# Performance work log

Measured on AMD Instinct MI355X. Metric: run time of the kernel, lower is better.

Reference implementation:

```python
import jax, jax.numpy as jnp
import numpy as np

N, E, IN, H, OUT = 100000, 600000, 128, 128, 64
BN_EPS = 1e-5


def setup_inputs() -> dict:
    key = jax.random.key(0)
    ks = jax.random.split(key, 8)
    def lin(k, i, o):
        return jax.random.normal(k, (i, o), jnp.float32) / np.float32(np.sqrt(i))
    return {
        "x": jax.random.normal(ks[0], (N, IN), jnp.float32),
        "edge_index": jax.random.randint(ks[1], (2, E), 0, N, dtype=jnp.int64),
        "W1": lin(ks[2], IN, H), "b1": jnp.zeros((H,), jnp.float32),
        "gamma": jnp.ones((H,), jnp.float32), "beta": jnp.zeros((H,), jnp.float32),
        "W2": lin(ks[3], H, H), "b2": jnp.zeros((H,), jnp.float32),
        "Wm1": lin(ks[4], H, H), "bm1": jnp.zeros((H,), jnp.float32),
        "Wm2": lin(ks[5], H, OUT), "bm2": jnp.zeros((OUT,), jnp.float32),
    }


def reference(x, edge_index, W1, b1, gamma, beta, W2, b2, Wm1, bm1, Wm2, bm2):
    # GINConv: h = MLP((1 + eps) * x + sum_{j in N(i)} x_j), eps = 0 (train_eps=False)
    src = edge_index[0]
    dst = edge_index[1]  # PyG aggregates messages at edge_index[1]
    agg = jax.ops.segment_sum(x[src], dst, num_segments=x.shape[0])  # [N, IN]
    h = agg + x
    # inner MLP: Linear -> BatchNorm (batch stats) -> ReLU -> Linear
    h = h @ W1 + b1
    mean = jnp.mean(h, axis=0)
    var = jnp.var(h, axis=0)
    h = (h - mean) * jax.lax.rsqrt(var + BN_EPS) * gamma + beta
    h = jax.nn.relu(h)
    h = h @ W2 + b2
    h = jax.nn.relu(h)  # .relu() after conv
    # output MLP (norm=None, dropout=0.5 -> identity at inference): Linear -> ReLU -> Linear
    h = jax.nn.relu(h @ Wm1 + bm1)
    return h @ Wm2 + bm2
```

## Files before the change

kernel.cpp:

```cpp
#include <hip/hip_runtime.h>
#include <hip/hip_bf16.h>
#include <stdint.h>

#define NNODES 100000
#define NEDGES 600000
#define SCAN_CHUNK 1024
#define SCAN_NB 98

typedef __attribute__((ext_vector_type(8))) short bf16x8;
typedef __attribute__((ext_vector_type(4))) float f32x4;
typedef __attribute__((ext_vector_type(4))) unsigned int u32x4;

__device__ inline float b2f(short b) {
    union { unsigned u; float f; } v;
    v.u = ((unsigned)(unsigned short)b) << 16;
    return v.f;
}
__device__ inline short f2b(float f) {
    union { float f; unsigned u; } v;
    v.f = f;
    unsigned r = (v.u + 0x7FFFu + ((v.u >> 16) & 1u)) >> 16;
    return (short)r;
}
__device__ inline unsigned packbf(float lo, float hi) {
    return ((unsigned)(unsigned short)f2b(hi) << 16) | (unsigned)(unsigned short)f2b(lo);
}
#define MFMA16(a, b, c) __builtin_amdgcn_mfma_f32_16x16x32_bf16(a, b, c, 0, 0, 0)

__device__ inline void stage_lds(const short* __restrict__ g, short* s, int w, int l, int n) {
#pragma unroll
    for (int i = 0; i < n; ++i) {
        int base = i * 4096 + w * 1024;
        __builtin_amdgcn_global_load_lds(
            (const __attribute__((address_space(1))) void*)((const char*)g + base + l * 16),
            (__attribute__((address_space(3))) void*)((char*)s + base), 16, 0, 0);
    }
}

__global__ __launch_bounds__(256) void k_prep(const float* __restrict__ x,
                                              const float* __restrict__ W1,
                                              const float* __restrict__ W2,
                                              const float* __restrict__ Wm1,
                                              const float* __restrict__ Wm2,
                                              short* __restrict__ xb, short* __restrict__ Wt,
                                              int* __restrict__ pos, float* __restrict__ stats) {
    int i = blockIdx.x * 256 + threadIdx.x;
    if (i < (NNODES + 1) * 16) {
        bf16x8 o = (bf16x8){0, 0, 0, 0, 0, 0, 0, 0};
        if (i < NNODES * 16) {
            const float4* p = (const float4*)(x + (size_t)i * 8);
            float4 a = p[0], b = p[1];
            o[0] = f2b(a.x); o[1] = f2b(a.y); o[2] = f2b(a.z); o[3] = f2b(a.w);
            o[4] = f2b(b.x); o[5] = f2b(b.y); o[6] = f2b(b.z); o[7] = f2b(b.w);
        }
        *(bf16x8*)(xb + (size_t)i * 8) = o;
    }
    if (i < NNODES) pos[i] = 0;
    if (i < 57344) {
        int jj, lane, kt, ct;
        const float* W;
        int ldw, off;
        if (i < 16384) { off = i; W = W1; ldw = 128; }
        else if (i < 32768) { off = i - 16384; W = W2; ldw = 128; }
        else if (i < 49152) { off = i - 32768; W = Wm1; ldw = 128; }
        else { off = i - 49152; W = Wm2; ldw = 64; }
        jj = off & 7;
        lane = (off >> 3) & 63;
        kt = (off >> 9) & 3;
        ct = (off >> 11) & 7;
        int lr = lane & 15, hi = lane >> 4;
        int c = ct * 16 + lr;
        int k = kt * 32 + hi * 8 + jj;
        Wt[i] = f2b(W[k * ldw + c]);
    }
    if (i < 256) stats[i] = 0.0f;
}


__global__ __launch_bounds__(256) void k_hist(const int* __restrict__ ei, int* __restrict__ cnt) {
    int e = blockIdx.x * 256 + threadIdx.x;
    if (e < NEDGES) atomicAdd(&cnt[ei[NEDGES + e]], 1);
}

__global__ __launch_bounds__(256) void k_scan1(const int* __restrict__ cnt, int* __restrict__ bsums) {
    __shared__ int sd[256];
    int b = blockIdx.x, t = threadIdx.x;
    int base = b * SCAN_CHUNK + t * 4;
    int s = 0;
#pragma unroll
    for (int i = 0; i < 4; ++i) {
        int idx = base + i;
        if (idx < NNODES) s += cnt[idx];
    }
    sd[t] = s;
    __syncthreads();
    for (int off = 128; off > 0; off >>= 1) {
        if (t < off) sd[t] += sd[t + off];
        __syncthreads();
    }
    if (t == 0) bsums[b] = sd[0];
}

__global__ __launch_bounds__(64) void k_scan2(int* __restrict__ bsums, int* __restrict__ rowptr) {
    if (threadIdx.x == 0 && blockIdx.x == 0) {
        int run = 0;
        for (int b = 0; b < SCAN_NB; ++b) {
            int v = bsums[b];
            bsums[b] = run;
            run += v;
        }
        rowptr[NNODES] = run;
    }
}

__global__ __launch_bounds__(256) void k_scan3(const int* __restrict__ cnt,
                                               const int* __restrict__ bsums,
                                               int* __restrict__ rowptr, int* __restrict__ pos) {
    __shared__ int sd[256];
    int b = blockIdx.x, t = threadIdx.x;
    int base = b * SCAN_CHUNK + t * 4;
    int v[4];
    int s = 0;
#pragma unroll
    for (int i = 0; i < 4; ++i) {
        int idx = base + i;
        v[i] = (idx < NNODES) ? cnt[idx] : 0;
        s += v[i];
    }
    sd[t] = s;
    __syncthreads();
    for (int off = 1; off < 256; off <<= 1) {
        int val = (t >= off) ? sd[t - off] : 0;
        __syncthreads();
        sd[t] += val;
        __syncthreads();
    }
    int run = sd[t] - s + bsums[b];
#pragma unroll
    for (int i = 0; i < 4; ++i) {
        int idx = base + i;
        if (idx < NNODES) {
            rowptr[idx] = run;
            pos[idx] = run;
            run += v[i];
        }
    }
}

__global__ __launch_bounds__(256) void k_fill(const int* __restrict__ ei, int* __restrict__ pos,
                                              int* __restrict__ elist) {
    int e = blockIdx.x * 256 + threadIdx.x;
    if (e >= NEDGES) return;
    int src = ei[e];
    int dst = ei[NEDGES + e];
    int p = atomicAdd(&pos[dst], 1);
    elist[p] = src;
}

__global__ __launch_bounds__(256) void k_agg(const short* __restrict__ xb,
                                             const int* __restrict__ rowptr,
                                             const int* __restrict__ elist,
                                             short* __restrict__ bufb) {
    int t = threadIdx.x;
    int w = t >> 6, lane = t & 63;
    int node = blockIdx.x * 4 + w;
    if (node >= NNODES) return;
    int beg = rowptr[node];
    int end = rowptr[node + 1];
    int deg = end - beg;
    int total = deg + 1;
    int sub = lane & 31, half = lane >> 5;
    const uint2* xr = (const uint2*)xb;

    float acc0 = 0.f, acc1 = 0.f, acc2 = 0.f, acc3 = 0.f;

    for (int base = 0; base < total; base += 64) {
        int j = base + lane;
        int ej = NNODES;
        if (j < total) ej = (j == 0) ? node : elist[beg + j - 1];
        int cnt = min(64, total - base);
        int pairs = (cnt + 1) >> 1;
        for (int i = 0; i < pairs; i += 4) {
            int j0 = 2 * i + half;
            int r0 = __shfl(ej, j0);
            int r1 = __shfl(ej, j0 + 2);
            int r2 = __shfl(ej, j0 + 4);
            int r3 = __shfl(ej, j0 + 6);
            uint2 v0 = xr[(size_t)r0 * 32 + sub];
            uint2 v1 = xr[(size_t)r1 * 32 + sub];
            uint2 v2 = xr[(size_t)r2 * 32 + sub];
            uint2 v3 = xr[(size_t)r3 * 32 + sub];
            acc0 += b2f((short)(v0.x & 0xFFFF)) + b2f((short)(v1.x & 0xFFFF)) +
                    b2f((short)(v2.x & 0xFFFF)) + b2f((short)(v3.x & 0xFFFF));
            acc1 += b2f((short)(v0.x >> 16)) + b2f((short)(v1.x >> 16)) +
                    b2f((short)(v2.x >> 16)) + b2f((short)(v3.x >> 16));
            acc2 += b2f((short)(v0.y & 0xFFFF)) + b2f((short)(v1.y & 0xFFFF)) +
                    b2f((short)(v2.y & 0xFFFF)) + b2f((short)(v3.y & 0xFFFF));
            acc3 += b2f((short)(v0.y >> 16)) + b2f((short)(v1.y >> 16)) +
                    b2f((short)(v2.y >> 16)) + b2f((short)(v3.y >> 16));
        }
    }
    acc0 += __shfl_xor(acc0, 32);
    acc1 += __shfl_xor(acc1, 32);
    acc2 += __shfl_xor(acc2, 32);
    acc3 += __shfl_xor(acc3, 32);
    if (half == 0) {
        uint2 o;
        o.x = ((uint32_t)(unsigned short)f2b(acc1) << 16) | (uint32_t)(unsigned short)f2b(acc0);
        o.y = ((uint32_t)(unsigned short)f2b(acc3) << 16) | (uint32_t)(unsigned short)f2b(acc2);
        ((uint2*)bufb)[(size_t)node * 32 + sub] = o;
    }
}

__global__ __launch_bounds__(256) void k_stats(const short* __restrict__ bufb,
                                               const short* __restrict__ W1pk,
                                               float* __restrict__ stats) {
    __shared__ float Sred[2][4][128];
    int t = threadIdx.x, w = t >> 6, l = t & 63;
    int r0 = blockIdx.x * 128;
    int row0 = (w & 1) * 64, col0 = (w >> 1) * 64;

    f32x4 acc[4][4];
#pragma unroll
    for (int r = 0; r < 4; ++r)
#pragma unroll
        for (int c = 0; c < 4; ++c) acc[r][c] = (f32x4){0.f, 0.f, 0.f, 0.f};

#pragma unroll
    for (int kb = 0; kb < 4; ++kb) {
        bf16x8 af[4], bw[4];
#pragma unroll
        for (int r = 0; r < 4; ++r)
            af[r] = *(const bf16x8*)(bufb + (size_t)(r0 + row0 + r * 16 + (l & 15)) * 128 +
                                     kb * 32 + (l >> 4) * 8);
#pragma unroll
        for (int c = 0; c < 4; ++c)
            bw[c] = *(const bf16x8*)(W1pk + ((((w >> 1) * 4 + c) * 4 + kb) * 64 + l) * 8);
#pragma unroll
        for (int r = 0; r < 4; ++r)
#pragma unroll
            for (int c = 0; c < 4; ++c) acc[r][c] = MFMA16(af[r], bw[c], acc[r][c]);
    }

    float s[4], q[4];
#pragma unroll
    for (int c = 0; c < 4; ++c) { s[c] = 0.f; q[c] = 0.f; }
#pragma unroll
    for (int c = 0; c < 4; ++c)
#pragma unroll
        for (int r = 0; r < 4; ++r)
#pragma unroll
            for (int rr = 0; rr < 4; ++rr) {
                int grow = r0 + row0 + r * 16 + (l >> 4) * 4 + rr;
                if (grow < NNODES) {
                    float v = acc[r][c][rr];
                    s[c] += v;
                    q[c] += v * v;
                }
            }
#pragma unroll
    for (int c = 0; c < 4; ++c) {
        s[c] += __shfl_xor(s[c], 16); s[c] += __shfl_xor(s[c], 32);
        q[c] += __shfl_xor(q[c], 16); q[c] += __shfl_xor(q[c], 32);
    }
    if (l < 16) {
#pragma unroll
        for (int c = 0; c < 4; ++c) {
            Sred[0][w][col0 + c * 16 + l] = s[c];
            Sred[1][w][col0 + c * 16 + l] = q[c];
        }
    }
    __syncthreads();
    if (t < 128) {
        int wb = (t < 64) ? 0 : 2;
        atomicAdd(stats + t, Sred[0][wb][t] + Sred[0][wb + 1][t]);
        atomicAdd(stats + 128 + t, Sred[1][wb][t] + Sred[1][wb + 1][t]);
    }
}

__global__ __launch_bounds__(256, 4) void k_mlp(const short* __restrict__ bufb,
                                                const float* __restrict__ stats,
                                                const float* __restrict__ gamma,
                                                const float* __restrict__ beta,
                                                const short* __restrict__ Wt,
                                                const float* __restrict__ b2,
                                                const float* __restrict__ bm1,
                                                const float* __restrict__ bm2,
                                                float* __restrict__ out) {
    __shared__ __align__(16) short wbuf[16384];
    __shared__ float scl[3][128], shf[3][128], bm2s[64];

    int t = threadIdx.x, w = t >> 6, l = t & 63;
    int lr = l & 15, hi = l >> 4;
    size_t node0 = (size_t)blockIdx.x * 128 + w * 32;

    stage_lds(Wt, wbuf, w, l, 8);
    if (t < 128) {
        float mean = stats[t] * (1.0f / NNODES);
        float var = fmaxf(stats[128 + t] * (1.0f / NNODES) - mean * mean, 0.0f);
        float inv = rsqrtf(var + 1e-5f);
        float sc = gamma[t] * inv;
        scl[0][t] = sc;
        shf[0][t] = beta[t] - mean * sc;
        scl[1][t] = 1.0f;
        shf[1][t] = b2[t];
        scl[2][t] = 1.0f;
        shf[2][t] = bm1[t];
    }
    if (t < 64) bm2s[t] = bm2[t];

    bf16x8 bvA[4], bvB[4];
#pragma unroll
    for (int kt = 0; kt < 4; ++kt) {
        bvA[kt] = *(const bf16x8*)(bufb + (node0 + lr) * 128 + kt * 32 + hi * 8);
        bvB[kt] = *(const bf16x8*)(bufb + (node0 + 16 + lr) * 128 + kt * 32 + hi * 8);
    }
    __syncthreads();

    unsigned pwA[8][2], pwB[8][2];

    for (int g = 0; g < 3; ++g) {
#pragma unroll
        for (int ch = 0; ch < 2; ++ch) {
            f32x4 aA[4], aB[4];
#pragma unroll
            for (int cc = 0; cc < 4; ++cc) {
                aA[cc] = (f32x4){0.f, 0.f, 0.f, 0.f};
                aB[cc] = (f32x4){0.f, 0.f, 0.f, 0.f};
            }
#pragma unroll
            for (int kt = 0; kt < 4; ++kt) {
                bf16x8 wv[4];
#pragma unroll
                for (int cc = 0; cc < 4; ++cc)
                    wv[cc] = *(const bf16x8*)(wbuf + ((((ch * 4 + cc) * 4) + kt) * 64 + l) * 8);
#pragma unroll
                for (int cc = 0; cc < 4; ++cc) {
                    aA[cc] = MFMA16(wv[cc], bvA[kt], aA[cc]);
                    aB[cc] = MFMA16(wv[cc], bvB[kt], aB[cc]);
                }
            }
#pragma unroll
            for (int cc = 0; cc < 4; ++cc) {
                int ct = ch * 4 + cc;
                int c0 = ct * 16 + hi * 4;
                float4 s4 = *(const float4*)&scl[g][c0];
                float4 h4 = *(const float4*)&shf[g][c0];
                pwA[ct][0] = packbf(fmaxf(aA[cc][0] * s4.x + h4.x, 0.f),
                                    fmaxf(aA[cc][1] * s4.y + h4.y, 0.f));
                pwA[ct][1] = packbf(fmaxf(aA[cc][2] * s4.z + h4.z, 0.f),
                                    fmaxf(aA[cc][3] * s4.w + h4.w, 0.f));
                pwB[ct][0] = packbf(fmaxf(aB[cc][0] * s4.x + h4.x, 0.f),
                                    fmaxf(aB[cc][1] * s4.y + h4.y, 0.f));
                pwB[ct][1] = packbf(fmaxf(aB[cc][2] * s4.z + h4.z, 0.f),
                                    fmaxf(aB[cc][3] * s4.w + h4.w, 0.f));
            }
        }
        __syncthreads();
        if (g < 2) stage_lds(Wt + (g + 1) * 16384, wbuf, w, l, 8);
        else       stage_lds(Wt + 49152, wbuf, w, l, 4);

        {
            int h2 = hi >> 1, h1 = hi & 1;
#pragma unroll
            for (int kt = 0; kt < 4; ++kt) {
                unsigned nwA[4], nwB[4];
#pragma unroll
                for (int jp = 0; jp < 4; ++jp) {
                    int srcl = (2 * h1 + (jp >> 1)) * 16 + lr;
                    unsigned veA = (unsigned)__shfl((int)pwA[2 * kt][jp & 1], srcl);
                    unsigned voA = (unsigned)__shfl((int)pwA[2 * kt + 1][jp & 1], srcl);
                    unsigned veB = (unsigned)__shfl((int)pwB[2 * kt][jp & 1], srcl);
                    unsigned voB = (unsigned)__shfl((int)pwB[2 * kt + 1][jp & 1], srcl);
                    nwA[jp] = h2 ? voA : veA;
                    nwB[jp] = h2 ? voB : veB;
                }
                u32x4 uqA = (u32x4){nwA[0], nwA[1], nwA[2], nwA[3]};
                u32x4 uqB = (u32x4){nwB[0], nwB[1], nwB[2], nwB[3]};
                bvA[kt] = __builtin_bit_cast(bf16x8, uqA);
                bvB[kt] = __builtin_bit_cast(bf16x8, uqB);
            }
        }
        __syncthreads();
    }

#pragma unroll
    for (int ct = 0; ct < 4; ++ct) {
        f32x4 aA = (f32x4){0.f, 0.f, 0.f, 0.f};
        f32x4 aB = (f32x4){0.f, 0.f, 0.f, 0.f};
#pragma unroll
        for (int kt = 0; kt < 4; ++kt) {
            bf16x8 wv = *(const bf16x8*)(wbuf + ((ct * 4 + kt) * 64 + l) * 8);
            aA = MFMA16(bvA[kt], wv, aA);
            aB = MFMA16(bvB[kt], wv, aB);
        }
        float bias = bm2s[ct * 16 + lr];
#pragma unroll
        for (int rr = 0; rr < 4; ++rr) {
            size_t growA = node0 + hi * 4 + rr;
            size_t growB = node0 + 16 + hi * 4 + rr;
            if (growA < NNODES) out[growA * 64 + ct * 16 + lr] = aA[rr] + bias;
            if (growB < NNODES) out[growB * 64 + ct * 16 + lr] = aB[rr] + bias;
        }
    }
}

extern "C" void kernel_launch(void* const* d_in, const int* in_sizes, int n_in,
                              void* d_out, int out_size, void* d_ws, size_t ws_size,
                              hipStream_t stream) {
    const float* x     = (const float*)d_in[0];
    const int*   ei    = (const int*)d_in[1];
    const float* W1    = (const float*)d_in[2];
    const float* gamma = (const float*)d_in[4];
    const float* beta  = (const float*)d_in[5];
    const float* W2    = (const float*)d_in[6];
    const float* b2    = (const float*)d_in[7];
    const float* Wm1   = (const float*)d_in[8];
    const float* bm1   = (const float*)d_in[9];
    const float* Wm2   = (const float*)d_in[10];
    const float* bm2   = (const float*)d_in[11];
    float* out = (float*)d_out;

    char* ws = (char*)d_ws;
    short* xb    = (short*)ws;
    short* bufb  = xb + (size_t)(NNODES + 1) * 128;
    short* Wt    = bufb + (size_t)(NNODES + 128) * 128;
    float* stats = (float*)(Wt + 57344);
    int* rowptr  = (int*)(stats + 256);
    int* pos     = rowptr + (NNODES + 1);
    int* elist   = pos + NNODES;
    int* bsums   = elist + NEDGES;

    int gE = (NEDGES + 255) / 256;
    int gPrep = ((NNODES + 1) * 16 + 255) / 256;

    k_prep<<<gPrep, 256, 0, stream>>>(x, W1, W2, Wm1, Wm2, xb, Wt, pos, stats);
    k_hist<<<gE, 256, 0, stream>>>(ei, pos);
    k_scan1<<<SCAN_NB, 256, 0, stream>>>(pos, bsums);
    k_scan2<<<1, 64, 0, stream>>>(bsums, rowptr);
    k_scan3<<<SCAN_NB, 256, 0, stream>>>(pos, bsums, rowptr, pos);
    k_fill<<<gE, 256, 0, stream>>>(ei, pos, elist);
    k_agg<<<(NNODES + 3) / 4, 256, 0, stream>>>(xb, rowptr, elist, bufb);

    int nblkS = (NNODES + 127) / 128;
    k_stats<<<nblkS, 256, 0, stream>>>(bufb, Wt, stats);
    int nblkM = (NNODES + 127) / 128;
    k_mlp<<<nblkM, 256, 0, stream>>>(bufb, stats, gamma, beta, Wt, b2, bm1, bm2, out);
}
```

Before: 172.1 us.

## Fuse neighbor aggregation with BatchNorm statistics GEMM via swizzled LDS tile

Merges the aggregation kernel and the batch-stats kernel into one. Each 512-thread block aggregates 64 nodes into a swizzled LDS tile, writes the tile to global memory, then runs the W1 MFMA and per-column sum and sum-of-squares reduction straight from LDS. This removes one launch and the re-read of the aggregated buffer from global memory. In exchange each block must finish its gather before any MFMA work starts, and the stats atomics are now issued per 64 rows instead of per 128.

```diff
diff --git a/kernel.cpp b/kernel.cpp
--- a/kernel.cpp
+++ b/kernel.cpp
@@ -24,6 +24,9 @@
 }
 __device__ inline unsigned packbf(float lo, float hi) {
     return ((unsigned)(unsigned short)f2b(hi) << 16) | (unsigned)(unsigned short)f2b(lo);
+}
+__device__ inline int swz(int row, int kbyte) {
+    return (row * 256 + kbyte) ^ ((row & 7) << 4);
 }
 #define MFMA16(a, b, c) __builtin_amdgcn_mfma_f32_16x16x32_bf16(a, b, c, 0, 0, 0)
 
@@ -157,124 +160,139 @@
     elist[p] = src;
 }
 
-__global__ __launch_bounds__(256) void k_agg(const short* __restrict__ xb,
-                                             const int* __restrict__ rowptr,
-                                             const int* __restrict__ elist,
-                                             short* __restrict__ bufb) {
-    int t = threadIdx.x;
-    int w = t >> 6, lane = t & 63;
-    int node = blockIdx.x * 4 + w;
-    if (node >= NNODES) return;
-    int beg = rowptr[node];
-    int end = rowptr[node + 1];
-    int deg = end - beg;
-    int total = deg + 1;
+__global__ __launch_bounds__(512, 8) void k_aggstats(const short* __restrict__ xb,
+                                                     const int* __restrict__ rowptr,
+                                                     const int* __restrict__ elist,
+                                                     const short* __restrict__ W1pk,
+                                                     short* __restrict__ bufb,
+                                                     float* __restrict__ stats) {
+    __shared__ __align__(16) short tile[64 * 128];
+    __shared__ float Sred[2][2][128];
+
+    int t = threadIdx.x, w = t >> 6, lane = t & 63;
     int sub = lane & 31, half = lane >> 5;
+    int node0 = blockIdx.x * 64;
     const uint2* xr = (const uint2*)xb;
 
-    float acc0 = 0.f, acc1 = 0.f, acc2 = 0.f, acc3 = 0.f;
-
-    for (int base = 0; base < total; base += 64) {
-        int j = base + lane;
-        int ej = NNODES;
-        if (j < total) ej = (j == 0) ? node : elist[beg + j - 1];
-        int cnt = min(64, total - base);
-        int pairs = (cnt + 1) >> 1;
-        for (int i = 0; i < pairs; i += 4) {
-            int j0 = 2 * i + half;
-            int r0 = __shfl(ej, j0);
-            int r1 = __shfl(ej, j0 + 2);
-            int r2 = __shfl(ej, j0 + 4);
-            int r3 = __shfl(ej, j0 + 6);
-            uint2 v0 = xr[(size_t)r0 * 32 + sub];
-            uint2 v1 = xr[(size_t)r1 * 32 + sub];
-            uint2 v2 = xr[(size_t)r2 * 32 + sub];
-            uint2 v3 = xr[(size_t)r3 * 32 + sub];
-            acc0 += b2f((short)(v0.x & 0xFFFF)) + b2f((short)(v1.x & 0xFFFF)) +
-                    b2f((short)(v2.x & 0xFFFF)) + b2f((short)(v3.x & 0xFFFF));
-            acc1 += b2f((short)(v0.x >> 16)) + b2f((short)(v1.x >> 16)) +
-                    b2f((short)(v2.x >> 16)) + b2f((short)(v3.x >> 16));
-            acc2 += b2f((short)(v0.y & 0xFFFF)) + b2f((short)(v1.y & 0xFFFF)) +
-                    b2f((short)(v2.y & 0xFFFF)) + b2f((short)(v3.y & 0xFFFF));
-            acc3 += b2f((short)(v0.y >> 16)) + b2f((short)(v1.y >> 16)) +
-                    b2f((short)(v2.y >> 16)) + b2f((short)(v3.y >> 16));
-        }
-    }
-    acc0 += __shfl_xor(acc0, 32);
-    acc1 += __shfl_xor(acc1, 32);
-    acc2 += __shfl_xor(acc2, 32);
-    acc3 += __shfl_xor(acc3, 32);
-    if (half == 0) {
-        uint2 o;
-        o.x = ((uint32_t)(unsigned short)f2b(acc1) << 16) | (uint32_t)(unsigned short)f2b(acc0);
-        o.y = ((uint32_t)(unsigned short)f2b(acc3) << 16) | (uint32_t)(unsigned short)f2b(acc2);
-        ((uint2*)bufb)[(size_t)node * 32 + sub] = o;
-    }
-}
-
-__global__ __launch_bounds__(256) void k_stats(const short* __restrict__ bufb,
-                                               const short* __restrict__ W1pk,
-                                               float* __restrict__ stats) {
-    __shared__ float Sred[2][4][128];
-    int t = threadIdx.x, w = t >> 6, l = t & 63;
-    int r0 = blockIdx.x * 128;
-    int row0 = (w & 1) * 64, col0 = (w >> 1) * 64;
-
-    f32x4 acc[4][4];
-#pragma unroll
-    for (int r = 0; r < 4; ++r)
-#pragma unroll
-        for (int c = 0; c < 4; ++c) acc[r][c] = (f32x4){0.f, 0.f, 0.f, 0.f};
-
-#pragma unroll
-    for (int kb = 0; kb < 4; ++kb) {
-        bf16x8 af[4], bw[4];
-#pragma unroll
-        for (int r = 0; r < 4; ++r)
-            af[r] = *(const bf16x8*)(bufb + (size_t)(r0 + row0 + r * 16 + (l & 15)) * 128 +
-                                     kb * 32 + (l >> 4) * 8);
-#pragma unroll
-        for (int c = 0; c < 4; ++c)
-            bw[c] = *(const bf16x8*)(W1pk + ((((w >> 1) * 4 + c) * 4 + kb) * 64 + l) * 8);
-#pragma unroll
-        for (int r = 0; r < 4; ++r)
-#pragma unroll
-            for (int c = 0; c < 4; ++c) acc[r][c] = MFMA16(af[r], bw[c], acc[r][c]);
-    }
-
-    float s[4], q[4];
-#pragma unroll
-    for (int c = 0; c < 4; ++c) { s[c] = 0.f; q[c] = 0.f; }
-#pragma unroll
-    for (int c = 0; c < 4; ++c)
-#pragma unroll
-        for (int r = 0; r < 4; ++r)
-#pragma unroll
-            for (int rr = 0; rr < 4; ++rr) {
-                int grow = r0 + row0 + r * 16 + (l >> 4) * 4 + rr;
-                if (grow < NNODES) {
+    int ridx = node0 + w * 8 + min(lane, 8);
+    int vr = rowptr[min(ridx, NNODES)];
+
+#pragma unroll
+    for (int i = 0; i < 8; ++i) {
+        int beg = __shfl(vr, i);
+        int end = __shfl(vr, i + 1);
+        int n = node0 + w * 8 + i;
+        float a0 = 0.f, a1 = 0.f, a2 = 0.f, a3 = 0.f;
+        if (n < NNODES) {
+            int total = end - beg + 1;
+            for (int base = 0; base < total; base += 64) {
+                int j = base + lane;
+                int ej = NNODES;
+                if (j < total) ej = (j == 0) ? n : elist[beg + j - 1];
+                int cnt = min(64, total - base);
+                int pairs = (cnt + 1) >> 1;
+                for (int ii = 0; ii < pairs; ii += 4) {
+                    int j0 = 2 * ii + half;
+                    int r0 = __shfl(ej, j0);
+                    int r1 = __shfl(ej, j0 + 2);
+                    int r2 = __shfl(ej, j0 + 4);
+                    int r3 = __shfl(ej, j0 + 6);
+                    uint2 v0 = xr[(size_t)r0 * 32 + sub];
+                    uint2 v1 = xr[(size_t)r1 * 32 + sub];
+                    uint2 v2 = xr[(size_t)r2 * 32 + sub];
+                    uint2 v3 = xr[(size_t)r3 * 32 + sub];
+                    a0 += b2f((short)(v0.x & 0xFFFF)) + b2f((short)(v1.x & 0xFFFF)) +
+                          b2f((short)(v2.x & 0xFFFF)) + b2f((short)(v3.x & 0xFFFF));
+                    a1 += b2f((short)(v0.x >> 16)) + b2f((short)(v1.x >> 16)) +
+                          b2f((short)(v2.x >> 16)) + b2f((short)(v3.x >> 16));
+                    a2 += b2f((short)(v0.y & 0xFFFF)) + b2f((short)(v1.y & 0xFFFF)) +
+                          b2f((short)(v2.y & 0xFFFF)) + b2f((short)(v3.y & 0xFFFF));
+                    a3 += b2f((short)(v0.y >> 16)) + b2f((short)(v1.y >> 16)) +
+                          b2f((short)(v2.y >> 16)) + b2f((short)(v3.y >> 16));
+                }
+            }
+        }
+        a0 += __shfl_xor(a0, 32);
+        a1 += __shfl_xor(a1, 32);
+        a2 += __shfl_xor(a2, 32);
+        a3 += __shfl_xor(a3, 32);
+        if (half == 0) {
+            int row = w * 8 + i;
+            int b8 = sub * 8;
+            int off = swz(row, b8 & ~15) + (b8 & 8);
+            uint2 o;
+            o.x = packbf(a0, a1);
+            o.y = packbf(a2, a3);
+            *(uint2*)((char*)tile + off) = o;
+        }
+    }
+    __syncthreads();
+
+    {
+        int row = t >> 3, chunk = t & 7;
+        int gr = node0 + row;
+        if (gr < NNODES) {
+            bf16x8 c0 = *(const bf16x8*)((char*)tile + swz(row, chunk * 32));
+            bf16x8 c1 = *(const bf16x8*)((char*)tile + swz(row, chunk * 32 + 16));
+            *(bf16x8*)(bufb + (size_t)gr * 128 + chunk * 16) = c0;
+            *(bf16x8*)(bufb + (size_t)gr * 128 + chunk * 16 + 8) = c1;
+        }
+    }
+
+    {
+        int lr = lane & 15, hi = lane >> 4;
+        int rg = w & 1, cg = w >> 1;
+        f32x4 acc[2][2];
+#pragma unroll
+        for (int r = 0; r < 2; ++r)
+#pragma unroll
+            for (int c = 0; c < 2; ++c) acc[r][c] = (f32x4){0.f, 0.f, 0.f, 0.f};
+#pragma unroll
+        for (int kb = 0; kb < 4; ++kb) {
+            int kbyte = kb * 64 + hi * 16;
+            bf16x8 af[2], bw[2];
+#pragma unroll
+            for (int r = 0; r < 2; ++r)
+                af[r] = *(const bf16x8*)((char*)tile + swz(rg * 32 + r * 16 + lr, kbyte));
+#pragma unroll
+            for (int c = 0; c < 2; ++c)
+                bw[c] = *(const bf16x8*)(W1pk + (((cg * 2 + c) * 4 + kb) * 64 + lane) * 8);
+#pragma unroll
+            for (int r = 0; r < 2; ++r)
+#pragma unroll
+                for (int c = 0; c < 2; ++c) acc[r][c] = MFMA16(af[r], bw[c], acc[r][c]);
+        }
+        float s[2], q[2];
+#pragma unroll
+        for (int c = 0; c < 2; ++c) { s[c] = 0.f; q[c] = 0.f; }
+#pragma unroll
+        for (int c = 0; c < 2; ++c)
+#pragma unroll
+            for (int r = 0; r < 2; ++r)
+#pragma unroll
+                for (int rr = 0; rr < 4; ++rr) {
                     float v = acc[r][c][rr];
                     s[c] += v;
                     q[c] += v * v;
                 }
-            }
-#pragma unroll
-    for (int c = 0; c < 4; ++c) {
-        s[c] += __shfl_xor(s[c], 16); s[c] += __shfl_xor(s[c], 32);
-        q[c] += __shfl_xor(q[c], 16); q[c] += __shfl_xor(q[c], 32);
-    }
-    if (l < 16) {
-#pragma unroll
-        for (int c = 0; c < 4; ++c) {
-            Sred[0][w][col0 + c * 16 + l] = s[c];
-            Sred[1][w][col0 + c * 16 + l] = q[c];
+#pragma unroll
+        for (int c = 0; c < 2; ++c) {
+            s[c] += __shfl_xor(s[c], 16); s[c] += __shfl_xor(s[c], 32);
+            q[c] += __shfl_xor(q[c], 16); q[c] += __shfl_xor(q[c], 32);
+        }
+        if (lane < 16) {
+#pragma unroll
+            for (int c = 0; c < 2; ++c) {
+                int col = (cg * 2 + c) * 16 + lane;
+                Sred[0][rg][col] = s[c];
+                Sred[1][rg][col] = q[c];
+            }
         }
     }
     __syncthreads();
     if (t < 128) {
-        int wb = (t < 64) ? 0 : 2;
-        atomicAdd(stats + t, Sred[0][wb][t] + Sred[0][wb + 1][t]);
-        atomicAdd(stats + 128 + t, Sred[1][wb][t] + Sred[1][wb + 1][t]);
+        atomicAdd(stats + t, Sred[0][0][t] + Sred[0][1][t]);
+        atomicAdd(stats + 128 + t, Sred[1][0][t] + Sred[1][1][t]);
     }
 }
 
@@ -440,10 +458,10 @@
     k_scan2<<<1, 64, 0, stream>>>(bsums, rowptr);
     k_scan3<<<SCAN_NB, 256, 0, stream>>>(pos, bsums, rowptr, pos);
     k_fill<<<gE, 256, 0, stream>>>(ei, pos, elist);
-    k_agg<<<(NNODES + 3) / 4, 256, 0, stream>>>(xb, rowptr, elist, bufb);
-
-    int nblkS = (NNODES + 127) / 128;
-    k_stats<<<nblkS, 256, 0, stream>>>(bufb, Wt, stats);
+
+    int gAgg = (NNODES + 63) / 64;
+    k_aggstats<<<gAgg, 512, 0, stream>>>(xb, rowptr, elist, Wt, bufb, stats);
+
     int nblkM = (NNODES + 127) / 128;
     k_mlp<<<nblkM, 256, 0, stream>>>(bufb, stats, gamma, beta, Wt, b2, bm1, bm2, out);
 }
```

Result: faster. 167.7 us (-2.5%).
